# Optimization experiments

Hardware: AMD Instinct MI355X
Metric: run time of the kernel (lower is better)

## Reference

```python
import jax, jax.numpy as jnp
import numpy as np

B, T, D, HD = 8, 2048, 768, 64

def setup_inputs() -> dict:
    key = jax.random.key(0)
    k1, k2, k3, k4 = jax.random.split(key, 4)
    scale = 1.0 / np.sqrt(D)
    return {
        "x": jax.random.normal(k1, (B, T, D), dtype=jnp.float32),
        "Wq": jax.random.normal(k2, (D, HD), dtype=jnp.float32) * scale,
        "Wk": jax.random.normal(k3, (D, HD), dtype=jnp.float32) * scale,
        "Wv": jax.random.normal(k4, (D, HD), dtype=jnp.float32) * scale,
    }

def reference(x, Wq, Wk, Wv):
    # q,k,v: [B,T,HD]
    q = jnp.einsum('btd,dh->bth', x, Wq)
    k = jnp.einsum('btd,dh->bth', x, Wk)
    v = jnp.einsum('btd,dh->bth', x, Wv)
    dk = q.shape[-1]
    # scores: [B,T,T], scaled then causally masked with -inf
    scores = jnp.einsum('bqh,bkh->bqk', q, k) / jnp.sqrt(jnp.float32(dk))
    Tq = scores.shape[-1]
    causal = jnp.tril(jnp.ones((Tq, Tq), dtype=bool))
    scores = jnp.where(causal, scores, -jnp.inf)
    attn = jax.nn.softmax(scores, axis=-1)  # dropout rate 0 (eval mode)
    return jnp.einsum('bqk,bkh->bqh', attn, v)
```

## Files before the change

### kernel.cpp

```cpp
#include <hip/hip_runtime.h>
#include <hip/hip_bf16.h>
#include <stdint.h>

#define B_  8
#define T_  2048
#define D_  768
#define HD_ 64
#define M_  (B_ * T_)

typedef short s16x8 __attribute__((ext_vector_type(8)));
typedef float f32x4 __attribute__((ext_vector_type(4)));
typedef float f32x16 __attribute__((ext_vector_type(16)));
typedef unsigned int u32;

union Frag { uint4 u; s16x8 h; };

__device__ __forceinline__ unsigned short f2bf(float f) {
    unsigned u = __builtin_bit_cast(unsigned, f);
    u += 0x7FFFu + ((u >> 16) & 1u);
    return (unsigned short)(u >> 16);
}
__device__ __forceinline__ unsigned pack_bf16x2(float lo, float hi) {
    return (unsigned)f2bf(lo) | ((unsigned)f2bf(hi) << 16);
}
__device__ __forceinline__ unsigned cvt_pk(float lo, float hi) {
    unsigned r;
    asm("v_cvt_pk_bf16_f32 %0, %1, %2" : "=v"(r) : "v"(lo), "v"(hi));
    return r;
}

__device__ __forceinline__ void gl_lds16(const void* g, void* l) {
    __builtin_amdgcn_global_load_lds(
        (const __attribute__((address_space(1))) u32*)g,
        (__attribute__((address_space(3))) u32*)l, 16, 0, 0);
}

__global__ __launch_bounds__(64) void prep_pk(const float* __restrict__ Wq,
                                              const float* __restrict__ Wk,
                                              const float* __restrict__ Wv,
                                              unsigned short* __restrict__ pk) {
    int nb = blockIdx.x / 24, kk = blockIdx.x % 24;
    int lane = threadIdx.x, g = lane >> 4, t = lane & 15;
    int mat = nb >> 2, col = (nb & 3) * 16 + t;
    const float* W = (mat == 0) ? Wq : (mat == 1) ? Wk : Wv;
    float s = (mat == 0) ? 0.18033688011112042f : 1.0f;
    float v[8];
#pragma unroll
    for (int e = 0; e < 8; e++)
        v[e] = W[(size_t)(kk * 32 + g * 8 + e) * HD_ + col] * s;
    uint4 u;
    u.x = pack_bf16x2(v[0], v[1]);
    u.y = pack_bf16x2(v[2], v[3]);
    u.z = pack_bf16x2(v[4], v[5]);
    u.w = pack_bf16x2(v[6], v[7]);
    *(uint4*)(pk + ((size_t)blockIdx.x * 64 + lane) * 8) = u;
}

__global__ __launch_bounds__(256, 2) void qkv_proj(const float* __restrict__ x,
                                                   const unsigned short* __restrict__ pk,
                                                   unsigned short* __restrict__ qo,
                                                   unsigned short* __restrict__ ko,
                                                   unsigned short* __restrict__ vt) {
    __shared__ char xs[4][8192];

    int tid = threadIdx.x, w = tid >> 6, lane = tid & 63;
    int g = lane >> 4, t = lane & 15;
    int m0 = blockIdx.x * 32;

    auto STAGE = [&](int jb) {
        int buf = jb & 3;
#pragma unroll
        for (int h = 0; h < 2; h++) {
            int s = tid + h * 256;
            int row = s >> 4;
            int a = (s & 15) ^ (row & 15);
            gl_lds16(x + (size_t)(m0 + row) * D_ + jb * 64 + a * 4,
                     &xs[buf][(w * 64 + h * 256) * 16]);
        }
    };

    const unsigned short* wp = pk + (size_t)w * 36864;
    auto LOADB = [&](Frag (&bb)[6], int jb) {
#pragma unroll
        for (int j = 0; j < 3; j++)
#pragma unroll
            for (int c = 0; c < 2; c++)
                bb[j * 2 + c].u = *(const uint4*)(wp + ((size_t)(j * 24 + jb * 2 + c) * 64 + lane) * 8);
    };

    f32x4 acc[3][2];
#pragma unroll
    for (int j = 0; j < 3; j++)
#pragma unroll
        for (int mf = 0; mf < 2; mf++) acc[j][mf] = (f32x4){0.f, 0.f, 0.f, 0.f};

    Frag bfr[3][6];
    LOADB(bfr[0], 0);
    LOADB(bfr[1], 1);
    STAGE(0); STAGE(1); STAGE(2);

#pragma unroll
    for (int jb = 0; jb < 12; jb++) {
        if (jb + 2 < 12) LOADB(bfr[(jb + 2) % 3], jb + 2);
        if (jb == 0)       asm volatile("s_waitcnt vmcnt(10)" ::: "memory");
        else if (jb == 10) asm volatile("s_waitcnt vmcnt(8)"  ::: "memory");
        else if (jb == 11) asm volatile("s_waitcnt vmcnt(0)"  ::: "memory");
        else               asm volatile("s_waitcnt vmcnt(16)" ::: "memory");
        __builtin_amdgcn_s_barrier();
        int buf = jb & 3;

        Frag af[2][2];
#pragma unroll
        for (int mf = 0; mf < 2; mf++) {
            int r32 = mf * 16 + t;
#pragma unroll
            for (int c = 0; c < 2; c++) {
                float4 f0 = *(const float4*)(&xs[buf][r32 * 256 + (((c * 8 + g * 2 + 0) ^ t) * 16)]);
                float4 f1 = *(const float4*)(&xs[buf][r32 * 256 + (((c * 8 + g * 2 + 1) ^ t) * 16)]);
                af[mf][c].u.x = cvt_pk(f0.x, f0.y);
                af[mf][c].u.y = cvt_pk(f0.z, f0.w);
                af[mf][c].u.z = cvt_pk(f1.x, f1.y);
                af[mf][c].u.w = cvt_pk(f1.z, f1.w);
            }
        }
        __builtin_amdgcn_s_setprio(1);
#pragma unroll
        for (int j = 0; j < 3; j++)
#pragma unroll
            for (int c = 0; c < 2; c++) {
                acc[j][0] = __builtin_amdgcn_mfma_f32_16x16x32_bf16(af[0][c].h, bfr[jb % 3][j * 2 + c].h, acc[j][0], 0, 0, 0);
                acc[j][1] = __builtin_amdgcn_mfma_f32_16x16x32_bf16(af[1][c].h, bfr[jb % 3][j * 2 + c].h, acc[j][1], 0, 0, 0);
            }
        __builtin_amdgcn_s_setprio(0);
        __builtin_amdgcn_s_barrier();
        if (jb + 3 < 12) STAGE(jb + 3);
    }

#pragma unroll
    for (int j = 0; j < 3; j++) {
        int nb = w * 3 + j;
        int col = (nb & 3) * 16 + t;
#pragma unroll
        for (int mf = 0; mf < 2; mf++) {
            int row0 = m0 + mf * 16;
            if (nb < 8) {
                unsigned short* dst = (nb < 4) ? qo : ko;
#pragma unroll
                for (int r = 0; r < 4; r++)
                    dst[(size_t)(row0 + g * 4 + r) * HD_ + col] = f2bf(acc[j][mf][r]);
            } else {
                int bb = m0 >> 11;
                int trow = (row0 & 2047) + g * 4;
                uint2 pkk;
                pkk.x = cvt_pk(acc[j][mf][0], acc[j][mf][1]);
                pkk.y = cvt_pk(acc[j][mf][2], acc[j][mf][3]);
                *(uint2*)(vt + (((size_t)(bb * HD_ + col)) << 11) + trow) = pkk;
            }
        }
    }
}

__global__ __launch_bounds__(256) void attn(const unsigned short* __restrict__ qw,
                                            const unsigned short* __restrict__ kw,
                                            const unsigned short* __restrict__ vt,
                                            float* __restrict__ out) {
    __shared__ char smem[65536];

    int tid = threadIdx.x, wv = tid >> 6, lane = tid & 63;
    int hi = lane >> 5, l31 = lane & 31;
    int blk = blockIdx.x;
    int b = blk & 7, idx = blk >> 3;
    int qblk = (idx < 32) ? (63 - idx) : (idx - 32);
    int q0 = qblk * 32;
    int qg = q0 + l31;
    size_t bbase = (size_t)b * T_;
    int nt = qblk + 1;
    int nq = (nt + 3) >> 2;

    const unsigned short* kp = kw + bbase * HD_;
    const unsigned short* vp = vt + ((size_t)(b * HD_) << 11);

    Frag qf[4];
#pragma unroll
    for (int c = 0; c < 4; c++)
        qf[c].u = *(const uint4*)(qw + (bbase + qg) * HD_ + c * 16 + hi * 8);

    auto STAGE = [&](int j) {
        int jj = (j < nt) ? j : (nt - 1);
        int kv0 = jj * 32, buf = j & 7;
        int kr = wv * 8 + (lane >> 3);
        int ka = (lane & 7) ^ (kr & 7);
        gl_lds16(kp + (size_t)(kv0 + kr) * HD_ + ka * 8, smem + buf * 4096 + wv * 1024);
        int vd = wv * 16 + (lane >> 2);
        int va = (lane & 3) ^ (vd & 3) ^ ((vd >> 2) & 3);
        gl_lds16(vp + ((size_t)vd << 11) + kv0 + va * 8, smem + 32768 + buf * 4096 + wv * 1024);
    };

    f32x16 o0, o1;
#pragma unroll
    for (int r = 0; r < 16; r++) { o0[r] = 0.f; o1[r] = 0.f; }
    float lacc = 0.f;

#pragma unroll
    for (int j0 = 0; j0 < 8; j0++) STAGE(j0);

#pragma unroll 1
    for (int i = 0; i < nq; i++) {
        asm volatile("s_waitcnt vmcnt(8)" ::: "memory");
        __builtin_amdgcn_s_barrier();
        int j = 4 * i + wv;
        if (j < nt) {
            const char* KB = smem + (j & 7) * 4096;
            const char* VB = smem + 32768 + (j & 7) * 4096;
            int kv0 = j * 32;
            f32x16 st;
#pragma unroll
            for (int r = 0; r < 16; r++) st[r] = 0.f;
            __builtin_amdgcn_s_setprio(1);
#pragma unroll
            for (int c = 0; c < 4; c++) {
                Frag ka;
                ka.u = *(const uint4*)(KB + l31 * 128 + (((c * 2 + hi) ^ (l31 & 7)) * 16));
                st = __builtin_amdgcn_mfma_f32_32x32x16_bf16(ka.h, qf[c].h, st, 0, 0, 0);
            }
            __builtin_amdgcn_s_setprio(0);

            if (j == qblk) {
#pragma unroll
                for (int r = 0; r < 16; r++) {
                    int key = kv0 + (r & 3) + 8 * (r >> 2) + 4 * hi;
                    if (key > qg) st[r] = -1e30f;
                }
            }

            float p[16], ss = 0.f;
#pragma unroll
            for (int r = 0; r < 16; r++) { p[r] = exp2f(st[r]); ss += p[r]; }
            lacc += ss;

            u32 A0 = cvt_pk(p[0], p[1]),   A1 = cvt_pk(p[2], p[3]);
            u32 B0 = cvt_pk(p[4], p[5]),   B1 = cvt_pk(p[6], p[7]);
            u32 C0 = cvt_pk(p[8], p[9]),   C1 = cvt_pk(p[10], p[11]);
            u32 D0 = cvt_pk(p[12], p[13]), D1 = cvt_pk(p[14], p[15]);
            u32 A0x = (u32)__shfl_xor((int)A0, 32);
            u32 A1x = (u32)__shfl_xor((int)A1, 32);
            u32 B0x = (u32)__shfl_xor((int)B0, 32);
            u32 B1x = (u32)__shfl_xor((int)B1, 32);
            u32 C0x = (u32)__shfl_xor((int)C0, 32);
            u32 C1x = (u32)__shfl_xor((int)C1, 32);
            u32 D0x = (u32)__shfl_xor((int)D0, 32);
            u32 D1x = (u32)__shfl_xor((int)D1, 32);
            Frag pf0, pf1;
            pf0.u.x = hi ? B0x : A0;
            pf0.u.y = hi ? B1x : A1;
            pf0.u.z = hi ? B0  : A0x;
            pf0.u.w = hi ? B1  : A1x;
            pf1.u.x = hi ? D0x : C0;
            pf1.u.y = hi ? D1x : C1;
            pf1.u.z = hi ? D0  : C0x;
            pf1.u.w = hi ? D1  : C1x;

            __builtin_amdgcn_s_setprio(1);
            {
                int sw0 = (l31 & 3) ^ ((l31 >> 2) & 3);
                Frag va;
                va.u = *(const uint4*)(VB + l31 * 64 + (((hi) ^ sw0) * 16));
                o0 = __builtin_amdgcn_mfma_f32_32x32x16_bf16(va.h, pf0.h, o0, 0, 0, 0);
                va.u = *(const uint4*)(VB + l31 * 64 + (((2 + hi) ^ sw0) * 16));
                o0 = __builtin_amdgcn_mfma_f32_32x32x16_bf16(va.h, pf1.h, o0, 0, 0, 0);
                int d1 = 32 + l31;
                int sw1 = (d1 & 3) ^ ((d1 >> 2) & 3);
                va.u = *(const uint4*)(VB + d1 * 64 + (((hi) ^ sw1) * 16));
                o1 = __builtin_amdgcn_mfma_f32_32x32x16_bf16(va.h, pf0.h, o1, 0, 0, 0);
                va.u = *(const uint4*)(VB + d1 * 64 + (((2 + hi) ^ sw1) * 16));
                o1 = __builtin_amdgcn_mfma_f32_32x32x16_bf16(va.h, pf1.h, o1, 0, 0, 0);
            }
            __builtin_amdgcn_s_setprio(0);
        }
        __builtin_amdgcn_s_barrier();
#pragma unroll
        for (int u = 0; u < 4; u++) STAGE(4 * i + 8 + u);
    }

    asm volatile("s_waitcnt vmcnt(0)" ::: "memory");
    __syncthreads();

    lacc += __shfl_xor(lacc, 32);
    float* MO = (float*)smem;
    if (wv) {
        int base = ((wv - 1) * 64 + lane) * 33;
#pragma unroll
        for (int r = 0; r < 16; r++) { MO[base + r] = o0[r]; MO[base + 16 + r] = o1[r]; }
        MO[base + 32] = lacc;
    }
    __syncthreads();
    if (wv == 0) {
        float ls = lacc;
#pragma unroll
        for (int k = 0; k < 3; k++) ls += MO[(k * 64 + lane) * 33 + 32];
        float inv = 1.0f / ls;
        float* op = out + (bbase + qg) * HD_;
#pragma unroll
        for (int r = 0; r < 16; r++) {
            float s0 = o0[r], s1 = o1[r];
#pragma unroll
            for (int k = 0; k < 3; k++) {
                s0 += MO[(k * 64 + lane) * 33 + r];
                s1 += MO[(k * 64 + lane) * 33 + 16 + r];
            }
            int dr = (r & 3) + 8 * (r >> 2) + 4 * hi;
            op[dr] = s0 * inv;
            op[32 + dr] = s1 * inv;
        }
    }
}

extern "C" void kernel_launch(void* const* d_in, const int* in_sizes, int n_in,
                              void* d_out, int out_size, void* d_ws, size_t ws_size,
                              hipStream_t stream) {
    const float* x  = (const float*)d_in[0];
    const float* Wq = (const float*)d_in[1];
    const float* Wk = (const float*)d_in[2];
    const float* Wv = (const float*)d_in[3];
    char* ws = (char*)d_ws;
    unsigned short* pkw = (unsigned short*)ws;
    unsigned short* qw = (unsigned short*)(ws + 294912);
    unsigned short* kw = (unsigned short*)(ws + 294912 + 2097152);
    unsigned short* vt = (unsigned short*)(ws + 294912 + 4194304);
    float* out = (float*)d_out;

    hipLaunchKernelGGL(prep_pk, dim3(288), dim3(64), 0, stream, Wq, Wk, Wv, pkw);
    hipLaunchKernelGGL(qkv_proj, dim3(M_ / 32), dim3(256), 0, stream, x, pkw, qw, kw, vt);
    hipLaunchKernelGGL(attn, dim3(512), dim3(256), 0, stream, qw, kw, vt, out);
}
```

Measured before the change: 49.21 us.

## Give each wave private double-buffered K/V staging and drop block barriers

Previously all four waves loaded K/V tiles together into a shared 8-slot LDS ring and met at two block barriers every iteration. Now each wave loads only the KV tiles it consumes (every fourth tile) into its own 16 KB LDS region, double-buffered, using only per-wave vmcnt waits. This removes block-wide barrier stalls and lets waves with different tile counts run at their own pace. In exchange, each wave issues four times more global-to-LDS loads per stage and prefetch is only two tiles deep per wave, so load latency may be less well hidden.

```diff
diff --git a/kernel.cpp b/kernel.cpp
--- a/kernel.cpp
+++ b/kernel.cpp
@@ -175,25 +175,32 @@
     int qg = q0 + l31;
     size_t bbase = (size_t)b * T_;
     int nt = qblk + 1;
-    int nq = (nt + 3) >> 2;
+    int ks = wv;
+    int mt = (nt > ks) ? ((nt - ks + 3) >> 2) : 0;
 
     const unsigned short* kp = kw + bbase * HD_;
     const unsigned short* vp = vt + ((size_t)(b * HD_) << 11);
+    char* KV = smem + wv * 16384;
 
     Frag qf[4];
 #pragma unroll
     for (int c = 0; c < 4; c++)
         qf[c].u = *(const uint4*)(qw + (bbase + qg) * HD_ + c * 16 + hi * 8);
 
-    auto STAGE = [&](int j) {
-        int jj = (j < nt) ? j : (nt - 1);
-        int kv0 = jj * 32, buf = j & 7;
-        int kr = wv * 8 + (lane >> 3);
-        int ka = (lane & 7) ^ (kr & 7);
-        gl_lds16(kp + (size_t)(kv0 + kr) * HD_ + ka * 8, smem + buf * 4096 + wv * 1024);
-        int vd = wv * 16 + (lane >> 2);
-        int va = (lane & 3) ^ (vd & 3) ^ ((vd >> 2) & 3);
-        gl_lds16(vp + ((size_t)vd << 11) + kv0 + va * 8, smem + 32768 + buf * 4096 + wv * 1024);
+    auto STAGE = [&](int j, int buf) {
+        int kv0 = j * 32;
+#pragma unroll
+        for (int q = 0; q < 4; q++) {
+            int kr = q * 8 + (lane >> 3);
+            int ka = (lane & 7) ^ (kr & 7);
+            gl_lds16(kp + (size_t)(kv0 + kr) * HD_ + ka * 8, KV + buf * 4096 + q * 1024);
+        }
+#pragma unroll
+        for (int q = 0; q < 4; q++) {
+            int vd = q * 16 + (lane >> 2);
+            int va = (lane & 3) ^ (vd & 3) ^ ((vd >> 2) & 3);
+            gl_lds16(vp + ((size_t)vd << 11) + kv0 + va * 8, KV + 8192 + buf * 4096 + q * 1024);
+        }
     };
 
     f32x16 o0, o1;
@@ -201,88 +208,85 @@
     for (int r = 0; r < 16; r++) { o0[r] = 0.f; o1[r] = 0.f; }
     float lacc = 0.f;
 
-#pragma unroll
-    for (int j0 = 0; j0 < 8; j0++) STAGE(j0);
+    if (mt > 0) STAGE(ks, 0);
+    if (mt > 1) STAGE(ks + 4, 1);
 
 #pragma unroll 1
-    for (int i = 0; i < nq; i++) {
-        asm volatile("s_waitcnt vmcnt(8)" ::: "memory");
-        __builtin_amdgcn_s_barrier();
-        int j = 4 * i + wv;
-        if (j < nt) {
-            const char* KB = smem + (j & 7) * 4096;
-            const char* VB = smem + 32768 + (j & 7) * 4096;
-            int kv0 = j * 32;
-            f32x16 st;
-#pragma unroll
-            for (int r = 0; r < 16; r++) st[r] = 0.f;
-            __builtin_amdgcn_s_setprio(1);
-#pragma unroll
-            for (int c = 0; c < 4; c++) {
-                Frag ka;
-                ka.u = *(const uint4*)(KB + l31 * 128 + (((c * 2 + hi) ^ (l31 & 7)) * 16));
-                st = __builtin_amdgcn_mfma_f32_32x32x16_bf16(ka.h, qf[c].h, st, 0, 0, 0);
-            }
-            __builtin_amdgcn_s_setprio(0);
-
-            if (j == qblk) {
-#pragma unroll
-                for (int r = 0; r < 16; r++) {
-                    int key = kv0 + (r & 3) + 8 * (r >> 2) + 4 * hi;
-                    if (key > qg) st[r] = -1e30f;
-                }
-            }
-
-            float p[16], ss = 0.f;
-#pragma unroll
-            for (int r = 0; r < 16; r++) { p[r] = exp2f(st[r]); ss += p[r]; }
-            lacc += ss;
-
-            u32 A0 = cvt_pk(p[0], p[1]),   A1 = cvt_pk(p[2], p[3]);
-            u32 B0 = cvt_pk(p[4], p[5]),   B1 = cvt_pk(p[6], p[7]);
-            u32 C0 = cvt_pk(p[8], p[9]),   C1 = cvt_pk(p[10], p[11]);
-            u32 D0 = cvt_pk(p[12], p[13]), D1 = cvt_pk(p[14], p[15]);
-            u32 A0x = (u32)__shfl_xor((int)A0, 32);
-            u32 A1x = (u32)__shfl_xor((int)A1, 32);
-            u32 B0x = (u32)__shfl_xor((int)B0, 32);
-            u32 B1x = (u32)__shfl_xor((int)B1, 32);
-            u32 C0x = (u32)__shfl_xor((int)C0, 32);
-            u32 C1x = (u32)__shfl_xor((int)C1, 32);
-            u32 D0x = (u32)__shfl_xor((int)D0, 32);
-            u32 D1x = (u32)__shfl_xor((int)D1, 32);
-            Frag pf0, pf1;
-            pf0.u.x = hi ? B0x : A0;
-            pf0.u.y = hi ? B1x : A1;
-            pf0.u.z = hi ? B0  : A0x;
-            pf0.u.w = hi ? B1  : A1x;
-            pf1.u.x = hi ? D0x : C0;
-            pf1.u.y = hi ? D1x : C1;
-            pf1.u.z = hi ? D0  : C0x;
-            pf1.u.w = hi ? D1  : C1x;
-
-            __builtin_amdgcn_s_setprio(1);
-            {
-                int sw0 = (l31 & 3) ^ ((l31 >> 2) & 3);
-                Frag va;
-                va.u = *(const uint4*)(VB + l31 * 64 + (((hi) ^ sw0) * 16));
-                o0 = __builtin_amdgcn_mfma_f32_32x32x16_bf16(va.h, pf0.h, o0, 0, 0, 0);
-                va.u = *(const uint4*)(VB + l31 * 64 + (((2 + hi) ^ sw0) * 16));
-                o0 = __builtin_amdgcn_mfma_f32_32x32x16_bf16(va.h, pf1.h, o0, 0, 0, 0);
-                int d1 = 32 + l31;
-                int sw1 = (d1 & 3) ^ ((d1 >> 2) & 3);
-                va.u = *(const uint4*)(VB + d1 * 64 + (((hi) ^ sw1) * 16));
-                o1 = __builtin_amdgcn_mfma_f32_32x32x16_bf16(va.h, pf0.h, o1, 0, 0, 0);
-                va.u = *(const uint4*)(VB + d1 * 64 + (((2 + hi) ^ sw1) * 16));
-                o1 = __builtin_amdgcn_mfma_f32_32x32x16_bf16(va.h, pf1.h, o1, 0, 0, 0);
-            }
-            __builtin_amdgcn_s_setprio(0);
-        }
-        __builtin_amdgcn_s_barrier();
-#pragma unroll
-        for (int u = 0; u < 4; u++) STAGE(4 * i + 8 + u);
-    }
-
-    asm volatile("s_waitcnt vmcnt(0)" ::: "memory");
+    for (int i = 0; i < mt; i++) {
+        if (i + 1 < mt) asm volatile("s_waitcnt vmcnt(8)" ::: "memory");
+        else            asm volatile("s_waitcnt vmcnt(0)" ::: "memory");
+        int j = ks + 4 * i;
+        const char* KB = KV + (i & 1) * 4096;
+        const char* VB = KV + 8192 + (i & 1) * 4096;
+        int kv0 = j * 32;
+
+        f32x16 st;
+#pragma unroll
+        for (int r = 0; r < 16; r++) st[r] = 0.f;
+        __builtin_amdgcn_s_setprio(1);
+#pragma unroll
+        for (int c = 0; c < 4; c++) {
+            Frag ka;
+            ka.u = *(const uint4*)(KB + l31 * 128 + (((c * 2 + hi) ^ (l31 & 7)) * 16));
+            st = __builtin_amdgcn_mfma_f32_32x32x16_bf16(ka.h, qf[c].h, st, 0, 0, 0);
+        }
+        __builtin_amdgcn_s_setprio(0);
+
+        if (j == qblk) {
+#pragma unroll
+            for (int r = 0; r < 16; r++) {
+                int key = kv0 + (r & 3) + 8 * (r >> 2) + 4 * hi;
+                if (key > qg) st[r] = -1e30f;
+            }
+        }
+
+        float p[16], ss = 0.f;
+#pragma unroll
+        for (int r = 0; r < 16; r++) { p[r] = exp2f(st[r]); ss += p[r]; }
+        lacc += ss;
+
+        u32 A0 = cvt_pk(p[0], p[1]),   A1 = cvt_pk(p[2], p[3]);
+        u32 B0 = cvt_pk(p[4], p[5]),   B1 = cvt_pk(p[6], p[7]);
+        u32 C0 = cvt_pk(p[8], p[9]),   C1 = cvt_pk(p[10], p[11]);
+        u32 D0 = cvt_pk(p[12], p[13]), D1 = cvt_pk(p[14], p[15]);
+        u32 A0x = (u32)__shfl_xor((int)A0, 32);
+        u32 A1x = (u32)__shfl_xor((int)A1, 32);
+        u32 B0x = (u32)__shfl_xor((int)B0, 32);
+        u32 B1x = (u32)__shfl_xor((int)B1, 32);
+        u32 C0x = (u32)__shfl_xor((int)C0, 32);
+        u32 C1x = (u32)__shfl_xor((int)C1, 32);
+        u32 D0x = (u32)__shfl_xor((int)D0, 32);
+        u32 D1x = (u32)__shfl_xor((int)D1, 32);
+        Frag pf0, pf1;
+        pf0.u.x = hi ? B0x : A0;
+        pf0.u.y = hi ? B1x : A1;
+        pf0.u.z = hi ? B0  : A0x;
+        pf0.u.w = hi ? B1  : A1x;
+        pf1.u.x = hi ? D0x : C0;
+        pf1.u.y = hi ? D1x : C1;
+        pf1.u.z = hi ? D0  : C0x;
+        pf1.u.w = hi ? D1  : C1x;
+
+        __builtin_amdgcn_s_setprio(1);
+        {
+            int sw0 = (l31 & 3) ^ ((l31 >> 2) & 3);
+            Frag va;
+            va.u = *(const uint4*)(VB + l31 * 64 + (((hi) ^ sw0) * 16));
+            o0 = __builtin_amdgcn_mfma_f32_32x32x16_bf16(va.h, pf0.h, o0, 0, 0, 0);
+            va.u = *(const uint4*)(VB + l31 * 64 + (((2 + hi) ^ sw0) * 16));
+            o0 = __builtin_amdgcn_mfma_f32_32x32x16_bf16(va.h, pf1.h, o0, 0, 0, 0);
+            int d1 = 32 + l31;
+            int sw1 = (d1 & 3) ^ ((d1 >> 2) & 3);
+            va.u = *(const uint4*)(VB + d1 * 64 + (((hi) ^ sw1) * 16));
+            o1 = __builtin_amdgcn_mfma_f32_32x32x16_bf16(va.h, pf0.h, o1, 0, 0, 0);
+            va.u = *(const uint4*)(VB + d1 * 64 + (((2 + hi) ^ sw1) * 16));
+            o1 = __builtin_amdgcn_mfma_f32_32x32x16_bf16(va.h, pf1.h, o1, 0, 0, 0);
+        }
+        __builtin_amdgcn_s_setprio(0);
+
+        if (i + 2 < mt) STAGE(ks + 4 * (i + 2), i & 1);
+    }
+
     __syncthreads();
 
     lacc += __shfl_xor(lacc, 32);
```

Result: faster. 45.13 us (-8.3%).
